# Performance work log

Measured on AMD Instinct MI355X. Metric: run time of the kernel, lower is better.

The kernel has to match this reference:

```python
import jax, jax.numpy as jnp
import numpy as np

B, C, H, W = 32, 64, 64, 64
K = 1024  # num_embeddings


def setup_inputs() -> dict:
    key = jax.random.key(0)
    k1, k2 = jax.random.split(key)
    inputs = jax.random.normal(k1, (B, C, H, W), dtype=jnp.float32)
    # codebook init: uniform(-1/K, 1/K) as in the torch module
    codebook = jax.random.uniform(k2, (K, C), dtype=jnp.float32,
                                  minval=-1.0 / K, maxval=1.0 / K)
    beta = jnp.float32(0.25)
    return {"inputs": inputs, "codebook": codebook, "beta": beta}


def reference(inputs, codebook, beta):
    sg = jax.lax.stop_gradient
    num_embeddings, dim = codebook.shape
    x = jnp.transpose(inputs, (0, 2, 3, 1))            # [B,H,W,C]
    flat = x.reshape(-1, dim)                          # [N,C]
    d = (jnp.sum(flat * flat, axis=1, keepdims=True)
         + jnp.sum(codebook * codebook, axis=1)
         - 2.0 * jnp.matmul(flat, codebook.T))         # [N,K]
    idx = jnp.argmin(d, axis=1)                        # [N] int
    # gather == one-hot @ codebook (same math, no one-hot materialized)
    quantized = codebook[idx].reshape(x.shape)         # [B,H,W,C]
    loss = (jnp.mean((sg(quantized) - x) ** 2)
            + beta * jnp.mean((quantized - sg(x)) ** 2))
    q_st = x + sg(quantized - x)                       # straight-through
    # codebook usage histogram -> perplexity
    counts = jnp.zeros((num_embeddings,), dtype=x.dtype).at[idx].add(1.0)
    e_mean = counts / flat.shape[0]
    perplexity = jnp.exp(-jnp.sum(e_mean * jnp.log(e_mean + 1e-10)))
    q_out = jnp.transpose(q_st, (0, 3, 1, 2))          # [B,C,H,W]
    return loss, q_out, perplexity
```

## Files before the change

### kernel.cpp

```cpp
#include <hip/hip_runtime.h>
#include <math.h>

constexpr int Cc  = 64;
constexpr int Kc  = 1024;
constexpr int HW  = 4096;
constexpr int CHW = Cc * HW;
constexpr int Nrows = 131072;
constexpr int TOTAL = 8388608;
constexpr int ROWS  = 64;
constexpr int NBLK  = Nrows / ROWS;

typedef __attribute__((ext_vector_type(8))) short short8;
typedef __attribute__((ext_vector_type(4))) float f32x4;

union U4S8 { uint4 u; short8 s; };

__device__ __forceinline__ unsigned bf16pair(float a, float b) {
    unsigned ua = __float_as_uint(a), ub = __float_as_uint(b);
    ua = (ua + 0x7FFFu + ((ua >> 16) & 1u)) >> 16;
    ub = (ub + 0x7FFFu + ((ub >> 16) & 1u)) & 0xFFFF0000u;
    return ua | ub;
}

__device__ __forceinline__ unsigned short bf16_rne(float x) {
    unsigned u = __float_as_uint(x);
    return (unsigned short)((u + 0x7FFFu + ((u >> 16) & 1u)) >> 16);
}

__device__ __forceinline__ unsigned umin3(unsigned a, unsigned b, unsigned c) {
    unsigned t = a < b ? a : b;
    return t < c ? t : c;
}

__global__ void prep_kernel(const float* __restrict__ cb,
                            float* __restrict__ e2p,
                            unsigned short* __restrict__ cbA,
                            unsigned int* __restrict__ counts) {
    int k = blockIdx.x;
    int c = threadIdx.x;
    float v = cb[k * Cc + c];
    float s = v * v;
    #pragma unroll
    for (int off = 32; off; off >>= 1) s += __shfl_down(s, off);
    if (c == 0) {
        e2p[k] = s;
        counts[k] = 0u;
    }
    int ct = k >> 4, n = k & 15;
    int ks = c >> 5, quad = (c >> 3) & 3, j = c & 7;
    cbA[(((ct * 2 + ks) * 64) + quad * 16 + n) * 8 + j] = bf16_rne(-v);
}

__global__ __launch_bounds__(256, 4) void vq_main(
        const float* __restrict__ inp,
        const float* __restrict__ cb,
        const float* __restrict__ e2p,
        const uint4* __restrict__ cbA4,
        float* __restrict__ qout,
        unsigned int* __restrict__ counts,
        float* __restrict__ bsum) {
    __shared__ uint4 lds_a[ROWS * 8];
    __shared__ unsigned lds_res[ROWS * 4];
    __shared__ float lds_x2w[4];

    const int tid = threadIdx.x;
    const int b   = blockIdx.x >> 6;
    const int hw0 = (blockIdx.x & 63) << 6;
    const int r   = tid & 63;
    const int w   = tid >> 6;
    const float* xp = inp + b * CHW + hw0 + r + w * 16 * HW;

    float x2 = 0.f;
    {
        float v[16];
        #pragma unroll
        for (int j = 0; j < 16; ++j) {
            v[j] = xp[j * HW];
            x2 = fmaf(v[j], v[j], x2);
        }
        uint4 p0, p1;
        p0.x = bf16pair(v[0],  v[1]);  p0.y = bf16pair(v[2],  v[3]);
        p0.z = bf16pair(v[4],  v[5]);  p0.w = bf16pair(v[6],  v[7]);
        p1.x = bf16pair(v[8],  v[9]);  p1.y = bf16pair(v[10], v[11]);
        p1.z = bf16pair(v[12], v[13]); p1.w = bf16pair(v[14], v[15]);
        lds_a[r * 8 + ((w * 2 + 0) ^ (r & 7))] = p0;
        lds_a[r * 8 + ((w * 2 + 1) ^ (r & 7))] = p1;
    }
    #pragma unroll
    for (int off = 32; off; off >>= 1) x2 += __shfl_down(x2, off);
    const int lane = tid & 63;
    if (lane == 0) lds_x2w[w] = x2;
    __syncthreads();

    const int col = lane & 15, quad = lane >> 4;

    short8 bf[4][2];
    #pragma unroll
    for (int nt = 0; nt < 4; ++nt) {
        int row = nt * 16 + col;
        #pragma unroll
        for (int ks = 0; ks < 2; ++ks) {
            U4S8 t; t.u = lds_a[row * 8 + ((ks * 4 + quad) ^ (row & 7))];
            bf[nt][ks] = t.s;
        }
    }

    unsigned best[4];
    #pragma unroll
    for (int nt = 0; nt < 4; ++nt) best[nt] = 0xFFFFFFFFu;

    unsigned c0 = (unsigned)(w * 256 + quad * 4);
    unsigned c1 = c0 + 1, c2 = c0 + 2, c3 = c0 + 3;

    const uint4* pc = cbA4 + (w * 16) * 128;
    uint4 pa0[2], pa1[2];
    pa0[0] = pc[lane];        pa1[0] = pc[64 + lane];
    pa0[1] = pc[128 + lane];  pa1[1] = pc[192 + lane];
    #pragma unroll 2
    for (int i = 0; i < 16; ++i) {
        U4S8 t0, t1; t0.u = pa0[i & 1]; t1.u = pa1[i & 1];
        int ni = (i + 2) & 15;
        pa0[i & 1] = pc[ni * 128 + lane];
        pa1[i & 1] = pc[ni * 128 + 64 + lane];

        #pragma unroll
        for (int nt = 0; nt < 4; ++nt) {
            f32x4 acc = {0.5f, 0.5f, 0.5f, 0.5f};
            acc = __builtin_amdgcn_mfma_f32_16x16x32_bf16(t0.s, bf[nt][0], acc, 0, 0, 0);
            acc = __builtin_amdgcn_mfma_f32_16x16x32_bf16(t1.s, bf[nt][1], acc, 0, 0, 0);
            unsigned k0 = (__float_as_uint(acc[0]) & 0xFFFFFC00u) | c0;
            unsigned k1 = (__float_as_uint(acc[1]) & 0xFFFFFC00u) | c1;
            unsigned k2 = (__float_as_uint(acc[2]) & 0xFFFFFC00u) | c2;
            unsigned k3 = (__float_as_uint(acc[3]) & 0xFFFFFC00u) | c3;
            best[nt] = umin3(best[nt], k0, k1);
            best[nt] = umin3(best[nt], k2, k3);
        }
        c0 += 16; c1 += 16; c2 += 16; c3 += 16;
    }

    #pragma unroll
    for (int nt = 0; nt < 4; ++nt) {
        unsigned v = best[nt];
        unsigned o = (unsigned)__shfl_xor((int)v, 16); v = v < o ? v : o;
        o = (unsigned)__shfl_xor((int)v, 32);          v = v < o ? v : o;
        if (quad == 0) lds_res[(nt * 16 + col) * 4 + w] = v;
    }
    __syncthreads();

    uint4 cand = *reinterpret_cast<const uint4*>(&lds_res[r * 4]);
    unsigned va = cand.x < cand.y ? cand.x : cand.y;
    unsigned vb = cand.z < cand.w ? cand.z : cand.w;
    unsigned vres = va < vb ? va : vb;
    int idx = (int)(vres & 1023u);

    const float4* qv = reinterpret_cast<const float4*>(cb + idx * Cc) + w * 4;
    float* op = qout + b * CHW + hw0 + r + w * 16 * HW;
    #pragma unroll
    for (int j = 0; j < 4; ++j) {
        float4 qq = qv[j];
        op[(j * 4 + 0) * HW] = qq.x;
        op[(j * 4 + 1) * HW] = qq.y;
        op[(j * 4 + 2) * HW] = qq.z;
        op[(j * 4 + 3) * HW] = qq.w;
    }

    if (tid < 64) {
        float dq = __uint_as_float(vres & 0xFFFFFC00u);
        float se = fmaf(2.0f, dq, e2p[idx] - 1.0f);
        atomicAdd(&counts[idx], 1u);
        #pragma unroll
        for (int off = 32; off; off >>= 1) se += __shfl_down(se, off);
        if (lane == 0) {
            float x2b = lds_x2w[0] + lds_x2w[1] + lds_x2w[2] + lds_x2w[3];
            bsum[blockIdx.x] = se + x2b;
        }
    }
}

__global__ void finalize_kernel(const unsigned int* __restrict__ counts,
                                const float* __restrict__ bsum,
                                const float* __restrict__ beta,
                                float* __restrict__ loss_out,
                                float* __restrict__ perp_out) {
    __shared__ float redp[16], reds[16];
    int t = threadIdx.x;
    float p = (float)counts[t] * (1.0f / (float)Nrows);
    float sp = p * logf(p + 1e-10f);
    float ss = bsum[t] + bsum[t + 1024];
    #pragma unroll
    for (int off = 32; off; off >>= 1) {
        sp += __shfl_down(sp, off);
        ss += __shfl_down(ss, off);
    }
    if ((t & 63) == 0) { redp[t >> 6] = sp; reds[t >> 6] = ss; }
    __syncthreads();
    if (t == 0) {
        float tp = 0.f, ts = 0.f;
        #pragma unroll
        for (int i = 0; i < 16; ++i) { tp += redp[i]; ts += reds[i]; }
        *perp_out = expf(-tp);
        *loss_out = (1.0f + *beta) * ts * (1.0f / (float)TOTAL);
    }
}

extern "C" void kernel_launch(void* const* d_in, const int* in_sizes, int n_in,
                              void* d_out, int out_size, void* d_ws, size_t ws_size,
                              hipStream_t stream) {
    const float* inp  = (const float*)d_in[0];
    const float* cb   = (const float*)d_in[1];
    const float* beta = (const float*)d_in[2];

    float* loss = (float*)d_out;
    float* qout = loss + 1;
    float* perp = loss + 1 + TOTAL;

    char* ws = (char*)d_ws;
    unsigned int* counts = (unsigned int*)ws;
    float* e2p  = (float*)(ws + 4096);
    float* bsum = (float*)(ws + 8192);
    unsigned short* cbA = (unsigned short*)(ws + 16384);

    prep_kernel<<<Kc, 64, 0, stream>>>(cb, e2p, cbA, counts);
    vq_main<<<NBLK, 256, 0, stream>>>(inp, cb, e2p, (const uint4*)cbA,
                                      qout, counts, bsum);
    finalize_kernel<<<1, Kc, 0, stream>>>(counts, bsum, beta, loss, perp);
}
```

Measured before the change: 122.1 us.

## Split VQ main kernel into index scan and separate quantized-output write kernel

The fused kernel is split in two. One kernel computes the nearest-codebook indices and stores them as 16-bit values in workspace. A second kernel gathers the codebook rows and writes the transposed quantized output. The aim is to take the large output store traffic out of the MFMA scan kernel so each kernel is simpler to schedule and needs fewer registers. The cost is an extra launch, an index buffer round-trip, and the loss of any overlap between compute and stores that the fused kernel had.

```diff
diff --git a/kernel.cpp b/kernel.cpp
--- a/kernel.cpp
+++ b/kernel.cpp
@@ -51,12 +51,11 @@
     cbA[(((ct * 2 + ks) * 64) + quad * 16 + n) * 8 + j] = bf16_rne(-v);
 }
 
-__global__ __launch_bounds__(256, 4) void vq_main(
+__global__ __launch_bounds__(256, 4) void vq_scan(
         const float* __restrict__ inp,
-        const float* __restrict__ cb,
         const float* __restrict__ e2p,
         const uint4* __restrict__ cbA4,
-        float* __restrict__ qout,
+        unsigned short* __restrict__ idx_out,
         unsigned int* __restrict__ counts,
         float* __restrict__ bsum) {
     __shared__ uint4 lds_a[ROWS * 8];
@@ -147,24 +146,13 @@
     }
     __syncthreads();
 
-    uint4 cand = *reinterpret_cast<const uint4*>(&lds_res[r * 4]);
-    unsigned va = cand.x < cand.y ? cand.x : cand.y;
-    unsigned vb = cand.z < cand.w ? cand.z : cand.w;
-    unsigned vres = va < vb ? va : vb;
-    int idx = (int)(vres & 1023u);
-
-    const float4* qv = reinterpret_cast<const float4*>(cb + idx * Cc) + w * 4;
-    float* op = qout + b * CHW + hw0 + r + w * 16 * HW;
-    #pragma unroll
-    for (int j = 0; j < 4; ++j) {
-        float4 qq = qv[j];
-        op[(j * 4 + 0) * HW] = qq.x;
-        op[(j * 4 + 1) * HW] = qq.y;
-        op[(j * 4 + 2) * HW] = qq.z;
-        op[(j * 4 + 3) * HW] = qq.w;
-    }
-
     if (tid < 64) {
+        uint4 cand = *reinterpret_cast<const uint4*>(&lds_res[r * 4]);
+        unsigned va = cand.x < cand.y ? cand.x : cand.y;
+        unsigned vb = cand.z < cand.w ? cand.z : cand.w;
+        unsigned vres = va < vb ? va : vb;
+        int idx = (int)(vres & 1023u);
+        idx_out[blockIdx.x * 64 + r] = (unsigned short)idx;
         float dq = __uint_as_float(vres & 0xFFFFFC00u);
         float se = fmaf(2.0f, dq, e2p[idx] - 1.0f);
         atomicAdd(&counts[idx], 1u);
@@ -174,6 +162,29 @@
             float x2b = lds_x2w[0] + lds_x2w[1] + lds_x2w[2] + lds_x2w[3];
             bsum[blockIdx.x] = se + x2b;
         }
+    }
+}
+
+__global__ __launch_bounds__(256, 4) void vq_write(
+        const float* __restrict__ cb,
+        const unsigned short* __restrict__ idx_in,
+        float* __restrict__ qout) {
+    const int t   = threadIdx.x;
+    const int b   = blockIdx.x >> 6;
+    const int hw0 = (blockIdx.x & 63) << 6;
+    const int hw  = t & 63;
+    const int cg  = t >> 6;
+
+    int idx = (int)idx_in[blockIdx.x * 64 + hw];
+    const float4* cb4 = reinterpret_cast<const float4*>(cb) + idx * 16 + cg * 4;
+    float* op = qout + b * CHW + (cg * 16) * HW + hw0 + hw;
+    #pragma unroll
+    for (int j = 0; j < 4; ++j) {
+        float4 q = cb4[j];
+        op[(j * 4 + 0) * HW] = q.x;
+        op[(j * 4 + 1) * HW] = q.y;
+        op[(j * 4 + 2) * HW] = q.z;
+        op[(j * 4 + 3) * HW] = q.w;
     }
 }
 
@@ -218,10 +229,12 @@
     unsigned int* counts = (unsigned int*)ws;
     float* e2p  = (float*)(ws + 4096);
     float* bsum = (float*)(ws + 8192);
-    unsigned short* cbA = (unsigned short*)(ws + 16384);
+    unsigned short* idxb = (unsigned short*)(ws + 16384);
+    unsigned short* cbA  = (unsigned short*)(ws + 278528);
 
     prep_kernel<<<Kc, 64, 0, stream>>>(cb, e2p, cbA, counts);
-    vq_main<<<NBLK, 256, 0, stream>>>(inp, cb, e2p, (const uint4*)cbA,
-                                      qout, counts, bsum);
+    vq_scan<<<NBLK, 256, 0, stream>>>(inp, e2p, (const uint4*)cbA,
+                                      idxb, counts, bsum);
+    vq_write<<<NBLK, 256, 0, stream>>>(cb, idxb, qout);
     finalize_kernel<<<1, Kc, 0, stream>>>(counts, bsum, beta, loss, perp);
 }
```

New measurement: 127.7 us. +4.6%, slower.
